# Kernel tuning notes

Measured on AMD Instinct MI355X. Metric: run time of the kernel, lower is better.

Reference implementation:

```python
import jax, jax.numpy as jnp
import numpy as np

B, N = 16, 512            # graphs per batch, nodes per graph
V, D_EMB = 100000, 64     # embedding table
F0 = 64                   # raw node feature width
H = 8                     # heads per layer
F_IN0 = F0 + D_EMB + 3    # 131 after concat(emb)+concat(user_emb)
O1, O2 = 128, 128         # f_out of layer 0 and 1
F_IN1 = H * O1            # 1024
EPS = 1e-5


def _xavier(key, shape):
    fan_in, fan_out = shape[-2], shape[-1]
    lim = float(np.sqrt(6.0 / (fan_in + fan_out)))
    return jax.random.uniform(key, shape, jnp.float32, -lim, lim)


def setup_inputs() -> dict:
    key = jax.random.key(0)
    ks = jax.random.split(key, 16)
    vertices = jax.random.randint(ks[0], (B, N), 0, V)
    adj = (jax.random.uniform(ks[1], (B, N, N)) < 0.1).astype(jnp.float32)
    adj = jnp.maximum(adj, jnp.eye(N, dtype=jnp.float32))  # self-loops: no empty softmax rows
    h = jax.random.normal(ks[2], (B, N, F0), jnp.float32)
    user_emb = jax.random.normal(ks[3], (B, N, 3), jnp.float32)
    emb_table = jax.random.normal(ks[4], (V, D_EMB), jnp.float32)
    return {
        "vertices": vertices, "adj": adj, "h": h, "user_emb": user_emb,
        "emb_table": emb_table,
        "norm1_w": jnp.ones((D_EMB,), jnp.float32), "norm1_b": jnp.zeros((D_EMB,), jnp.float32),
        "norm2_w": jnp.ones((3,), jnp.float32), "norm2_b": jnp.zeros((3,), jnp.float32),
        "w0": _xavier(ks[5], (H, F_IN0, O1)),
        "a_src0": _xavier(ks[6], (H, O1, 1)), "a_dst0": _xavier(ks[7], (H, O1, 1)),
        "w1": _xavier(ks[8], (H, F_IN1, O2)),
        "a_src1": _xavier(ks[9], (H, O2, 1)), "a_dst1": _xavier(ks[10], (H, O2, 1)),
    }


def _instance_norm(x, w, b):
    # torch InstanceNorm1d on x.transpose(1,2): normalize over node dim per (batch, channel)
    mu = jnp.mean(x, axis=1, keepdims=True)
    var = jnp.var(x, axis=1, keepdims=True)  # biased variance, as torch
    return (x - mu) * jax.lax.rsqrt(var + EPS) * w + b


def _gat_layer(h, adj, w, a_src, a_dst):
    # h: [b,n,f_in], w: [h,f_in,o]
    hp = jnp.einsum('bnf,hfo->bhno', h, w)            # h_prime
    t = jnp.tanh(hp)
    s = jnp.einsum('bhno,ho->bhn', t, a_src[..., 0])  # attn_src
    d = jnp.einsum('bhno,ho->bhn', t, a_dst[..., 0])  # attn_dst
    attn = s[:, :, :, None] + d[:, :, None, :]        # [b,h,n,n]
    attn = jnp.where(attn >= 0, attn, 0.2 * attn)     # leaky_relu(0.2)
    attn = jnp.where(adj[:, None, :, :] > 0, attn, -jnp.inf)
    attn = jax.nn.softmax(attn, axis=-1)              # (dropout is identity in eval)
    return jnp.einsum('bhnm,bhmo->bhno', attn, hp)


def reference(vertices, adj, h, user_emb, emb_table,
              norm1_w, norm1_b, norm2_w, norm2_b,
              w0, a_src0, a_dst0, w1, a_src1, a_dst1):
    emb = emb_table[vertices]                         # [b,n,D_EMB]
    emb = _instance_norm(emb, norm1_w, norm1_b)
    x = jnp.concatenate([h, emb], axis=2)
    ue = _instance_norm(user_emb, norm2_w, norm2_b)
    x = jnp.concatenate([x, ue], axis=2)              # [b,n,F_IN0]
    # layer 0 (not last): elu + head concat
    x = _gat_layer(x, adj, w0, a_src0, a_dst0)        # [b,H,n,O1]
    x = jax.nn.elu(jnp.transpose(x, (0, 2, 1, 3)).reshape(B, N, H * O1))
    # layer 1 (last): mean over heads
    x = _gat_layer(x, adj, w1, a_src1, a_dst1)        # [b,H,n,O2]
    x = jnp.mean(x, axis=1)                           # [b,n,O2]
    return jax.nn.log_softmax(x, axis=-1)
```

## Files before the change

### kernel.cpp

```cpp
#include <hip/hip_runtime.h>
#include <hip/hip_bf16.h>
#include <cmath>

#define B_  16
#define N_  512
#define H_  8
#define F0_ 64
#define DEMB_ 64
#define FIN0_ 131
#define KP0_ 192
#define O_  128
#define FIN1_ 1024
#define LOG2E_ 1.4426950408889634f

typedef __attribute__((ext_vector_type(4))) float f32x4;
typedef __attribute__((ext_vector_type(8))) short bf16x8;

__device__ inline ushort f2bf(float f) {
    union { float f; unsigned u; } x; x.f = f;
    unsigned r = x.u + 0x7fff + ((x.u >> 16) & 1);
    return (ushort)(r >> 16);
}
__device__ inline float bf2f(ushort u) {
    union { unsigned u; float f; } x; x.u = ((unsigned)u) << 16;
    return x.f;
}
__device__ inline float tanh_fast(float x) {
    x = fminf(fmaxf(x, -15.f), 15.f);
    float e = __expf(2.f * x);
    return (e - 1.f) * __frcp_rn(e + 1.f);
}

__global__ __launch_bounds__(256) void k_copy_h(const float* __restrict__ h,
                                                ushort* __restrict__ x0) {
    int i = blockIdx.x * 256 + threadIdx.x;
    int r = i >> 6, c = i & 63;
    x0[(size_t)r * KP0_ + c] = f2bf(h[i]);
    x0[(size_t)r * KP0_ + 128 + c] = 0;
}

__global__ __launch_bounds__(256) void k_emb_norm(const int* __restrict__ verts,
                                                  const float* __restrict__ table,
                                                  const float* __restrict__ w,
                                                  const float* __restrict__ bb,
                                                  ushort* __restrict__ x0) {
    int b = blockIdx.x >> 6, c = blockIdx.x & 63;
    int t = threadIdx.x;
    float vals[2], sum = 0.f, sq = 0.f;
#pragma unroll
    for (int i = 0; i < 2; ++i) {
        int n = t + i * 256;
        int vid = verts[b * N_ + n];
        float v = table[(size_t)vid * DEMB_ + c];
        vals[i] = v; sum += v; sq += v * v;
    }
    __shared__ float s0[256], s1[256];
    s0[t] = sum; s1[t] = sq; __syncthreads();
    for (int o = 128; o > 0; o >>= 1) {
        if (t < o) { s0[t] += s0[t + o]; s1[t] += s1[t + o]; }
        __syncthreads();
    }
    float mu = s0[0] * (1.f / N_);
    float var = s1[0] * (1.f / N_) - mu * mu;
    float inv = rsqrtf(var + 1e-5f);
    float ww = w[c], bv = bb[c];
#pragma unroll
    for (int i = 0; i < 2; ++i) {
        int n = t + i * 256;
        x0[((size_t)b * N_ + n) * KP0_ + 64 + c] = f2bf((vals[i] - mu) * inv * ww + bv);
    }
}

__global__ __launch_bounds__(256) void k_ue_norm(const float* __restrict__ ue,
                                                 const float* __restrict__ w,
                                                 const float* __restrict__ bb,
                                                 ushort* __restrict__ x0) {
    int b = blockIdx.x / 3, c = blockIdx.x % 3;
    int t = threadIdx.x;
    float vals[2], sum = 0.f, sq = 0.f;
#pragma unroll
    for (int i = 0; i < 2; ++i) {
        int n = t + i * 256;
        float v = ue[((size_t)b * N_ + n) * 3 + c];
        vals[i] = v; sum += v; sq += v * v;
    }
    __shared__ float s0[256], s1[256];
    s0[t] = sum; s1[t] = sq; __syncthreads();
    for (int o = 128; o > 0; o >>= 1) {
        if (t < o) { s0[t] += s0[t + o]; s1[t] += s1[t + o]; }
        __syncthreads();
    }
    float mu = s0[0] * (1.f / N_);
    float var = s1[0] * (1.f / N_) - mu * mu;
    float inv = rsqrtf(var + 1e-5f);
    float ww = w[c], bv = bb[c];
#pragma unroll
    for (int i = 0; i < 2; ++i) {
        int n = t + i * 256;
        x0[((size_t)b * N_ + n) * KP0_ + 128 + c] = f2bf((vals[i] - mu) * inv * ww + bv);
    }
}

__global__ __launch_bounds__(128) void k_wt_all(const float* __restrict__ w0,
                                                const float* __restrict__ w1,
                                                ushort* __restrict__ wt0,
                                                ushort* __restrict__ wt1) {
    int bid = blockIdx.x;
    int o = threadIdx.x;
    if (bid < 192) {
        int hh = bid / 24, kc = bid % 24;
        bf16x8 v;
#pragma unroll
        for (int j = 0; j < 8; ++j) {
            int k = kc * 8 + j;
            float f = (k < FIN0_) ? w0[((size_t)hh * FIN0_ + k) * 128 + o] : 0.f;
            v[j] = (short)f2bf(f);
        }
        *(bf16x8*)(wt0 + ((size_t)(hh * 128 + o)) * KP0_ + kc * 8) = v;
    } else {
        int b2 = bid - 192;
        int hh = b2 >> 7, kc = b2 & 127;
        bf16x8 v;
#pragma unroll
        for (int j = 0; j < 8; ++j) {
            int k = kc * 8 + j;
            float f = w1[((size_t)hh * FIN1_ + k) * 128 + o];
            v[j] = (short)f2bf(f);
        }
        *(bf16x8*)(wt1 + ((size_t)(hh * 128 + o)) * FIN1_ + kc * 8) = v;
    }
}

__global__ __launch_bounds__(256) void k_mask(const float* __restrict__ adj,
                                              unsigned long long* __restrict__ mask) {
    int gid = blockIdx.x * 256 + threadIdx.x;
    float v = adj[gid];
    unsigned long long m = __ballot(v > 0.f);
    if ((threadIdx.x & 63) == 0) mask[gid >> 6] = m;
}

template <int K>
__global__ __launch_bounds__(256, 2) void k_gemm(const ushort* __restrict__ A,
                                                 const ushort* __restrict__ Wt,
                                                 const float* __restrict__ asrc,
                                                 const float* __restrict__ adst,
                                                 ushort* __restrict__ hpT,
                                                 float* __restrict__ sout,
                                                 float* __restrict__ dout) {
    __shared__ ushort As[128 * 64];
    __shared__ ushort Bs[128 * 64];
    int bid = blockIdx.x;
    int hh = bid & 7;
    int mt = bid >> 3;
    int tid = threadIdx.x;
    int wid = tid >> 6, l = tid & 63;
    int wm = wid >> 1, wn = wid & 1;

    const ushort* Ab = A + (size_t)mt * 128 * K;
    const ushort* Wb = Wt + (size_t)hh * 128 * K;

    f32x4 acc[4][4];
#pragma unroll
    for (int m = 0; m < 4; ++m)
#pragma unroll
        for (int n = 0; n < 4; ++n) acc[m][n] = (f32x4){0.f, 0.f, 0.f, 0.f};

    int srow = tid >> 3;
    int segp = tid & 7;

    for (int kt = 0; kt < K / 64; ++kt) {
        int k0 = kt * 64;
#pragma unroll
        for (int it = 0; it < 4; ++it) {
            int row = it * 32 + srow;
            int segl = segp ^ (row & 7);
            size_t goff = (size_t)row * K + k0 + segl * 8;
            int loff = (it * 32 + wid * 8) * 64;
            __builtin_amdgcn_global_load_lds(
                (const __attribute__((address_space(1))) void*)(Ab + goff),
                (__attribute__((address_space(3))) void*)(As + loff), 16, 0, 0);
            __builtin_amdgcn_global_load_lds(
                (const __attribute__((address_space(1))) void*)(Wb + goff),
                (__attribute__((address_space(3))) void*)(Bs + loff), 16, 0, 0);
        }
        __syncthreads();

        int lr = l & 15;
        int kg = l >> 4;
#pragma unroll
        for (int kk = 0; kk < 2; ++kk) {
            int segl = kk * 4 + kg;
            bf16x8 a[4], b[4];
#pragma unroll
            for (int m = 0; m < 4; ++m) {
                int row = wm * 64 + m * 16 + lr;
                int sp = segl ^ (row & 7);
                a[m] = *(const bf16x8*)(As + row * 64 + sp * 8);
            }
#pragma unroll
            for (int n = 0; n < 4; ++n) {
                int row = wn * 64 + n * 16 + lr;
                int sp = segl ^ (row & 7);
                b[n] = *(const bf16x8*)(Bs + row * 64 + sp * 8);
            }
#pragma unroll
            for (int m = 0; m < 4; ++m)
#pragma unroll
                for (int n = 0; n < 4; ++n)
                    acc[m][n] = __builtin_amdgcn_mfma_f32_16x16x32_bf16(a[m], b[n], acc[m][n], 0, 0, 0);
        }
        __syncthreads();
    }

    int bb = mt >> 2;
    int n_in_b = (mt & 3) * 128;
    int bh = bb * H_ + hh;
    ushort* Hp = hpT + ((size_t)bh * 128) * 512;
#pragma unroll
    for (int m = 0; m < 4; ++m)
#pragma unroll
        for (int n = 0; n < 4; ++n) {
            int rr = wm * 64 + m * 16 + (l >> 4) * 4;
            int cc = wn * 64 + n * 16 + (l & 15);
            ushort4 v;
            v.x = f2bf(acc[m][n][0]);
            v.y = f2bf(acc[m][n][1]);
            v.z = f2bf(acc[m][n][2]);
            v.w = f2bf(acc[m][n][3]);
            *(ushort4*)(Hp + (size_t)cc * 512 + n_in_b + rr) = v;
        }

    float* sP = (float*)As;
    float* dP = sP + 256;
    float av[4], dv[4];
#pragma unroll
    for (int n = 0; n < 4; ++n) {
        int cc = wn * 64 + n * 16 + (l & 15);
        av[n] = asrc[hh * 128 + cc];
        dv[n] = adst[hh * 128 + cc];
    }
#pragma unroll
    for (int m = 0; m < 4; ++m)
#pragma unroll
        for (int j = 0; j < 4; ++j) {
            float sv = 0.f, dvv = 0.f;
#pragma unroll
            for (int n = 0; n < 4; ++n) {
                float th = tanh_fast(acc[m][n][j]);
                sv += th * av[n];
                dvv += th * dv[n];
            }
#pragma unroll
            for (int off = 1; off < 16; off <<= 1) {
                sv += __shfl_xor(sv, off);
                dvv += __shfl_xor(dvv, off);
            }
            if ((l & 15) == 0) {
                int rr = wm * 64 + m * 16 + (l >> 4) * 4 + j;
                sP[wn * 128 + rr] = sv;
                dP[wn * 128 + rr] = dvv;
            }
        }
    __syncthreads();
    if (tid < 128) {
        sout[(size_t)bh * 512 + n_in_b + tid] = (sP[tid] + sP[128 + tid]) * LOG2E_;
    } else {
        int r = tid - 128;
        dout[(size_t)bh * 512 + n_in_b + r] = (dP[r] + dP[128 + r]) * LOG2E_;
    }
}

template <bool L0>
__global__ __launch_bounds__(256, 2) void k_attn(const ushort* __restrict__ hpT,
                                                 const float* __restrict__ sbuf,
                                                 const float* __restrict__ dbuf,
                                                 const unsigned* __restrict__ mask32,
                                                 ushort* __restrict__ out) {
    __shared__ ushort Vbuf[128 * 64];
    __shared__ ushort Abuf[128 * 64];
    __shared__ float dsh[512];
    __shared__ float rsh[128];

    int bid = blockIdx.x;
    int xcd = bid & 7, idx = bid >> 3;
    int bh = xcd + 8 * (idx & 15);
    int tile = idx >> 4;
    int b = bh >> 3, hh = bh & 7;
    int n0 = tile * 128;
    int t = threadIdx.x;
    int wid = t >> 6, l = t & 63;
    int wm = wid >> 1, wn = wid & 1;
    int lr = l & 15, kg = l >> 4;

    const ushort* Vb = hpT + (size_t)bh * 128 * 512;

    int row = t >> 1, mh = t & 1;
    float sv = sbuf[(size_t)bh * 512 + n0 + row];
    unsigned mw[8];
#pragma unroll
    for (int c = 0; c < 8; ++c)
        mw[c] = mask32[((size_t)(b * 512 + n0 + row) << 4) + c * 2 + mh];

    dsh[t] = dbuf[(size_t)bh * 512 + t];
    dsh[256 + t] = dbuf[(size_t)bh * 512 + 256 + t];
    __syncthreads();

    f32x4 acc[4][4];
#pragma unroll
    for (int m = 0; m < 4; ++m)
#pragma unroll
        for (int n = 0; n < 4; ++n) acc[m][n] = (f32x4){0.f, 0.f, 0.f, 0.f};

    float rsum = 0.f;
    int srow = t >> 3, segp = t & 7;

#pragma unroll
    for (int c = 0; c < 8; ++c) {
        int m0 = c * 64;
#pragma unroll
        for (int it = 0; it < 4; ++it) {
            int rrow = it * 32 + srow;
            int segl = segp ^ (rrow & 7);
            __builtin_amdgcn_global_load_lds(
                (const __attribute__((address_space(1))) void*)(Vb + (size_t)rrow * 512 + m0 + segl * 8),
                (__attribute__((address_space(3))) void*)(Vbuf + (it * 32 + wid * 8) * 64),
                16, 0, 0);
        }

        const float* dp = dsh + m0 + mh * 32;
        unsigned mwc = mw[c];
#pragma unroll
        for (int j = 0; j < 4; ++j) {
            f32x4 da = *(const f32x4*)(dp + j * 8);
            f32x4 db2 = *(const f32x4*)(dp + j * 8 + 4);
            float ev[8];
#pragma unroll
            for (int q = 0; q < 8; ++q) {
                float dm = (q < 4) ? da[q] : db2[q - 4];
                float lg = sv + dm;
                lg = fmaxf(lg, 0.2f * lg);
                float e = ((mwc >> (j * 8 + q)) & 1) ? exp2f(lg) : 0.f;
                rsum += e;
                ev[q] = e;
            }
            unsigned p01, p23, p45, p67;
            asm("v_cvt_pk_bf16_f32 %0, %1, %2" : "=v"(p01) : "v"(ev[0]), "v"(ev[1]));
            asm("v_cvt_pk_bf16_f32 %0, %1, %2" : "=v"(p23) : "v"(ev[2]), "v"(ev[3]));
            asm("v_cvt_pk_bf16_f32 %0, %1, %2" : "=v"(p45) : "v"(ev[4]), "v"(ev[5]));
            asm("v_cvt_pk_bf16_f32 %0, %1, %2" : "=v"(p67) : "v"(ev[6]), "v"(ev[7]));
            int s = mh * 4 + j;
            int phys = s ^ (row & 7);
            uint4 pk4 = {p01, p23, p45, p67};
            *(uint4*)((char*)Abuf + row * 128 + phys * 16) = pk4;
        }
        __syncthreads();

#pragma unroll
        for (int kk = 0; kk < 2; ++kk) {
            int s = kk * 4 + kg;
            bf16x8 a[4], bfr[4];
#pragma unroll
            for (int m = 0; m < 4; ++m) {
                int rw = wm * 64 + m * 16 + lr;
                int sp = s ^ (rw & 7);
                a[m] = *(const bf16x8*)(Vbuf + rw * 64 + sp * 8);
            }
#pragma unroll
            for (int n = 0; n < 4; ++n) {
                int rw = wn * 64 + n * 16 + lr;
                int sp = s ^ (rw & 7);
                bfr[n] = *(const bf16x8*)(Abuf + rw * 64 + sp * 8);
            }
#pragma unroll
            for (int m = 0; m < 4; ++m)
#pragma unroll
                for (int n = 0; n < 4; ++n)
                    acc[m][n] = __builtin_amdgcn_mfma_f32_16x16x32_bf16(a[m], bfr[n], acc[m][n], 0, 0, 0);
        }
        __syncthreads();
    }

    rsum += __shfl_xor(rsum, 1);
    if ((t & 1) == 0) rsh[row] = rsum;
    __syncthreads();

#pragma unroll
    for (int n = 0; n < 4; ++n) {
        int nn = wn * 64 + n * 16 + lr;
        float ri = __frcp_rn(rsh[nn]);
        size_t orow;
        if (L0)
            orow = ((size_t)(b * 512 + n0 + nn)) * FIN1_ + hh * 128;
        else
            orow = ((size_t)bh * 512 + n0 + nn) * 128;
#pragma unroll
        for (int m = 0; m < 4; ++m) {
            int o0 = wm * 64 + m * 16 + kg * 4;
            f32x4 v = acc[m][n];
            ushort4 w;
            float f0 = v[0] * ri, f1 = v[1] * ri, f2 = v[2] * ri, f3 = v[3] * ri;
            if (L0) {
                f0 = (f0 > 0.f) ? f0 : expm1f(f0);
                f1 = (f1 > 0.f) ? f1 : expm1f(f1);
                f2 = (f2 > 0.f) ? f2 : expm1f(f2);
                f3 = (f3 > 0.f) ? f3 : expm1f(f3);
            }
            w.x = f2bf(f0); w.y = f2bf(f1); w.z = f2bf(f2); w.w = f2bf(f3);
            *(ushort4*)(out + orow + o0) = w;
        }
    }
}

__global__ __launch_bounds__(128) void k_out(const ushort* __restrict__ o1,
                                             float* __restrict__ out) {
    int row = blockIdx.x;
    int b = row >> 9, n = row & 511;
    int t = threadIdx.x;
    float v = 0.f;
#pragma unroll
    for (int hh = 0; hh < H_; ++hh)
        v += bf2f(o1[((size_t)(b * H_ + hh) * N_ + n) * O_ + t]);
    v *= 0.125f;
    float m = v;
#pragma unroll
    for (int off = 32; off > 0; off >>= 1) m = fmaxf(m, __shfl_down(m, off));
    __shared__ float red[4];
    if ((t & 63) == 0) red[t >> 6] = m;
    __syncthreads();
    float rm = fmaxf(red[0], red[1]);
    float e = __expf(v - rm);
    float ss = e;
#pragma unroll
    for (int off = 32; off > 0; off >>= 1) ss += __shfl_down(ss, off);
    if ((t & 63) == 0) red[2 + (t >> 6)] = ss;
    __syncthreads();
    float rs2 = red[2] + red[3];
    out[(size_t)row * O_ + t] = v - rm - logf(rs2);
}

extern "C" void kernel_launch(void* const* d_in, const int* in_sizes, int n_in,
                              void* d_out, int out_size, void* d_ws, size_t ws_size,
                              hipStream_t stream) {
    const int*   verts = (const int*)d_in[0];
    const float* adj   = (const float*)d_in[1];
    const float* h     = (const float*)d_in[2];
    const float* ue    = (const float*)d_in[3];
    const float* table = (const float*)d_in[4];
    const float* n1w   = (const float*)d_in[5];
    const float* n1b   = (const float*)d_in[6];
    const float* n2w   = (const float*)d_in[7];
    const float* n2b   = (const float*)d_in[8];
    const float* w0    = (const float*)d_in[9];
    const float* as0   = (const float*)d_in[10];
    const float* ad0   = (const float*)d_in[11];
    const float* w1    = (const float*)d_in[12];
    const float* as1   = (const float*)d_in[13];
    const float* ad1   = (const float*)d_in[14];
    float* out = (float*)d_out;

    ushort* x0p  = (ushort*)d_ws;
    ushort* wt0  = x0p + 1572864;
    ushort* wt1  = wt0 + 196608;
    ushort* hpT  = wt1 + 1048576;
    ushort* x1bf = hpT + 8388608;
    ushort* o1   = x1bf + 8388608;
    unsigned long long* mask = (unsigned long long*)(o1 + 8388608);
    float* sb = (float*)(mask + 65536);
    float* db = sb + 65536;

    hipLaunchKernelGGL(k_copy_h,   dim3(2048), dim3(256), 0, stream, h, x0p);
    hipLaunchKernelGGL(k_emb_norm, dim3(1024), dim3(256), 0, stream, verts, table, n1w, n1b, x0p);
    hipLaunchKernelGGL(k_ue_norm,  dim3(48),   dim3(256), 0, stream, ue, n2w, n2b, x0p);
    hipLaunchKernelGGL(k_wt_all,   dim3(1216), dim3(128), 0, stream, w0, w1, wt0, wt1);
    hipLaunchKernelGGL(k_mask,     dim3(16384), dim3(256), 0, stream, adj, mask);

    hipLaunchKernelGGL((k_gemm<KP0_>), dim3(512), dim3(256), 0, stream,
                       x0p, wt0, as0, ad0, hpT, sb, db);
    hipLaunchKernelGGL((k_attn<true>), dim3(512), dim3(256), 0, stream,
                       hpT, sb, db, (const unsigned*)mask, x1bf);

    hipLaunchKernelGGL((k_gemm<FIN1_>), dim3(512), dim3(256), 0, stream,
                       x1bf, wt1, as1, ad1, hpT, sb, db);
    hipLaunchKernelGGL((k_attn<false>), dim3(512), dim3(256), 0, stream,
                       hpT, sb, db, (const unsigned*)mask, o1);

    hipLaunchKernelGGL(k_out, dim3(8192), dim3(128), 0, stream, o1, out);
}
```

Before: 142.1 us.

## Fuse preprocessing kernels, remap GEMM blocks, halve attention query tile

Merges the five preprocessing launches (feature copy, embedding norm, user-emb norm, weight transpose, mask build) into one kernel that branches on block index, removing launch gaps. The GEMM block order now groups M-tiles per XCD so neighbouring blocks share a head's weight tile. Attention drops to 64 query rows per block with four threads per row, doubling the grid to 1024 blocks for better occupancy and load balance. The cost is that each attention block reloads the V tile for half as many queries, and the fused preprocess kernel is a single large grid with divergent block roles.

After: 117.2 us. -17.6%, faster.

```diff
diff --git a/kernel.cpp b/kernel.cpp
--- a/kernel.cpp
+++ b/kernel.cpp
@@ -31,112 +31,110 @@
     return (e - 1.f) * __frcp_rn(e + 1.f);
 }
 
-__global__ __launch_bounds__(256) void k_copy_h(const float* __restrict__ h,
-                                                ushort* __restrict__ x0) {
-    int i = blockIdx.x * 256 + threadIdx.x;
-    int r = i >> 6, c = i & 63;
-    x0[(size_t)r * KP0_ + c] = f2bf(h[i]);
-    x0[(size_t)r * KP0_ + 128 + c] = 0;
-}
-
-__global__ __launch_bounds__(256) void k_emb_norm(const int* __restrict__ verts,
-                                                  const float* __restrict__ table,
-                                                  const float* __restrict__ w,
-                                                  const float* __restrict__ bb,
-                                                  ushort* __restrict__ x0) {
-    int b = blockIdx.x >> 6, c = blockIdx.x & 63;
+__global__ __launch_bounds__(256) void k_pre(const float* __restrict__ h,
+                                             const int* __restrict__ verts,
+                                             const float* __restrict__ table,
+                                             const float* __restrict__ n1w,
+                                             const float* __restrict__ n1b,
+                                             const float* __restrict__ ue,
+                                             const float* __restrict__ n2w,
+                                             const float* __restrict__ n2b,
+                                             const float* __restrict__ w0,
+                                             const float* __restrict__ w1,
+                                             const float* __restrict__ adj,
+                                             ushort* __restrict__ x0,
+                                             ushort* __restrict__ wt0,
+                                             ushort* __restrict__ wt1,
+                                             unsigned long long* __restrict__ mask) {
+    __shared__ float s0[256], s1[256];
+    int bid = blockIdx.x;
     int t = threadIdx.x;
-    float vals[2], sum = 0.f, sq = 0.f;
-#pragma unroll
-    for (int i = 0; i < 2; ++i) {
-        int n = t + i * 256;
-        int vid = verts[b * N_ + n];
-        float v = table[(size_t)vid * DEMB_ + c];
-        vals[i] = v; sum += v; sq += v * v;
-    }
-    __shared__ float s0[256], s1[256];
-    s0[t] = sum; s1[t] = sq; __syncthreads();
-    for (int o = 128; o > 0; o >>= 1) {
-        if (t < o) { s0[t] += s0[t + o]; s1[t] += s1[t + o]; }
-        __syncthreads();
-    }
-    float mu = s0[0] * (1.f / N_);
-    float var = s1[0] * (1.f / N_) - mu * mu;
-    float inv = rsqrtf(var + 1e-5f);
-    float ww = w[c], bv = bb[c];
-#pragma unroll
-    for (int i = 0; i < 2; ++i) {
-        int n = t + i * 256;
-        x0[((size_t)b * N_ + n) * KP0_ + 64 + c] = f2bf((vals[i] - mu) * inv * ww + bv);
-    }
-}
-
-__global__ __launch_bounds__(256) void k_ue_norm(const float* __restrict__ ue,
-                                                 const float* __restrict__ w,
-                                                 const float* __restrict__ bb,
-                                                 ushort* __restrict__ x0) {
-    int b = blockIdx.x / 3, c = blockIdx.x % 3;
-    int t = threadIdx.x;
-    float vals[2], sum = 0.f, sq = 0.f;
-#pragma unroll
-    for (int i = 0; i < 2; ++i) {
-        int n = t + i * 256;
-        float v = ue[((size_t)b * N_ + n) * 3 + c];
-        vals[i] = v; sum += v; sq += v * v;
-    }
-    __shared__ float s0[256], s1[256];
-    s0[t] = sum; s1[t] = sq; __syncthreads();
-    for (int o = 128; o > 0; o >>= 1) {
-        if (t < o) { s0[t] += s0[t + o]; s1[t] += s1[t + o]; }
-        __syncthreads();
-    }
-    float mu = s0[0] * (1.f / N_);
-    float var = s1[0] * (1.f / N_) - mu * mu;
-    float inv = rsqrtf(var + 1e-5f);
-    float ww = w[c], bv = bb[c];
-#pragma unroll
-    for (int i = 0; i < 2; ++i) {
-        int n = t + i * 256;
-        x0[((size_t)b * N_ + n) * KP0_ + 128 + c] = f2bf((vals[i] - mu) * inv * ww + bv);
-    }
-}
-
-__global__ __launch_bounds__(128) void k_wt_all(const float* __restrict__ w0,
-                                                const float* __restrict__ w1,
-                                                ushort* __restrict__ wt0,
-                                                ushort* __restrict__ wt1) {
-    int bid = blockIdx.x;
-    int o = threadIdx.x;
-    if (bid < 192) {
-        int hh = bid / 24, kc = bid % 24;
-        bf16x8 v;
-#pragma unroll
-        for (int j = 0; j < 8; ++j) {
-            int k = kc * 8 + j;
-            float f = (k < FIN0_) ? w0[((size_t)hh * FIN0_ + k) * 128 + o] : 0.f;
-            v[j] = (short)f2bf(f);
-        }
-        *(bf16x8*)(wt0 + ((size_t)(hh * 128 + o)) * KP0_ + kc * 8) = v;
+
+    if (bid < 2048) {
+        int i = bid * 256 + t;
+        int r = i >> 6, c = i & 63;
+        x0[(size_t)r * KP0_ + c] = f2bf(h[i]);
+        if (c >= 3) x0[(size_t)r * KP0_ + 128 + c] = 0;
+    } else if (bid < 3072) {
+        int b2 = bid - 2048;
+        int b = b2 >> 6, c = b2 & 63;
+        float vals[2], sum = 0.f, sq = 0.f;
+#pragma unroll
+        for (int i = 0; i < 2; ++i) {
+            int n = t + i * 256;
+            int vid = verts[b * N_ + n];
+            float v = table[(size_t)vid * DEMB_ + c];
+            vals[i] = v; sum += v; sq += v * v;
+        }
+        s0[t] = sum; s1[t] = sq; __syncthreads();
+        for (int o = 128; o > 0; o >>= 1) {
+            if (t < o) { s0[t] += s0[t + o]; s1[t] += s1[t + o]; }
+            __syncthreads();
+        }
+        float mu = s0[0] * (1.f / N_);
+        float var = s1[0] * (1.f / N_) - mu * mu;
+        float inv = rsqrtf(var + 1e-5f);
+        float ww = n1w[c], bv = n1b[c];
+#pragma unroll
+        for (int i = 0; i < 2; ++i) {
+            int n = t + i * 256;
+            x0[((size_t)b * N_ + n) * KP0_ + 64 + c] = f2bf((vals[i] - mu) * inv * ww + bv);
+        }
+    } else if (bid < 3120) {
+        int b3 = bid - 3072;
+        int b = b3 / 3, c = b3 % 3;
+        float vals[2], sum = 0.f, sq = 0.f;
+#pragma unroll
+        for (int i = 0; i < 2; ++i) {
+            int n = t + i * 256;
+            float v = ue[((size_t)b * N_ + n) * 3 + c];
+            vals[i] = v; sum += v; sq += v * v;
+        }
+        s0[t] = sum; s1[t] = sq; __syncthreads();
+        for (int o = 128; o > 0; o >>= 1) {
+            if (t < o) { s0[t] += s0[t + o]; s1[t] += s1[t + o]; }
+            __syncthreads();
+        }
+        float mu = s0[0] * (1.f / N_);
+        float var = s1[0] * (1.f / N_) - mu * mu;
+        float inv = rsqrtf(var + 1e-5f);
+        float ww = n2w[c], bv = n2b[c];
+#pragma unroll
+        for (int i = 0; i < 2; ++i) {
+            int n = t + i * 256;
+            x0[((size_t)b * N_ + n) * KP0_ + 128 + c] = f2bf((vals[i] - mu) * inv * ww + bv);
+        }
+    } else if (bid < 3728) {
+        int ob = (bid - 3120) * 2 + (t >> 7);
+        int o = t & 127;
+        if (ob < 192) {
+            int hh = ob / 24, kc = ob % 24;
+            bf16x8 v;
+#pragma unroll
+            for (int j = 0; j < 8; ++j) {
+                int k = kc * 8 + j;
+                float f = (k < FIN0_) ? w0[((size_t)hh * FIN0_ + k) * 128 + o] : 0.f;
+                v[j] = (short)f2bf(f);
+            }
+            *(bf16x8*)(wt0 + ((size_t)(hh * 128 + o)) * KP0_ + kc * 8) = v;
+        } else {
+            int b2 = ob - 192;
+            int hh = b2 >> 7, kc = b2 & 127;
+            bf16x8 v;
+#pragma unroll
+            for (int j = 0; j < 8; ++j) {
+                int k = kc * 8 + j;
+                float f = w1[((size_t)hh * FIN1_ + k) * 128 + o];
+                v[j] = (short)f2bf(f);
+            }
+            *(bf16x8*)(wt1 + ((size_t)(hh * 128 + o)) * FIN1_ + kc * 8) = v;
+        }
     } else {
-        int b2 = bid - 192;
-        int hh = b2 >> 7, kc = b2 & 127;
-        bf16x8 v;
-#pragma unroll
-        for (int j = 0; j < 8; ++j) {
-            int k = kc * 8 + j;
-            float f = w1[((size_t)hh * FIN1_ + k) * 128 + o];
-            v[j] = (short)f2bf(f);
-        }
-        *(bf16x8*)(wt1 + ((size_t)(hh * 128 + o)) * FIN1_ + kc * 8) = v;
-    }
-}
-
-__global__ __launch_bounds__(256) void k_mask(const float* __restrict__ adj,
-                                              unsigned long long* __restrict__ mask) {
-    int gid = blockIdx.x * 256 + threadIdx.x;
-    float v = adj[gid];
-    unsigned long long m = __ballot(v > 0.f);
-    if ((threadIdx.x & 63) == 0) mask[gid >> 6] = m;
+        int gid = (bid - 3728) * 256 + t;
+        float v = adj[gid];
+        unsigned long long m = __ballot(v > 0.f);
+        if ((t & 63) == 0) mask[gid >> 6] = m;
+    }
 }
 
 template <int K>
@@ -150,8 +148,9 @@
     __shared__ ushort As[128 * 64];
     __shared__ ushort Bs[128 * 64];
     int bid = blockIdx.x;
-    int hh = bid & 7;
-    int mt = bid >> 3;
+    int idx = bid >> 3;
+    int mt = (bid & 7) + 8 * (idx & 7);
+    int hh = idx >> 3;
     int tid = threadIdx.x;
     int wid = tid >> 6, l = tid & 63;
     int wm = wid >> 1, wn = wid & 1;
@@ -277,16 +276,16 @@
                                                  const unsigned* __restrict__ mask32,
                                                  ushort* __restrict__ out) {
     __shared__ ushort Vbuf[128 * 64];
-    __shared__ ushort Abuf[128 * 64];
+    __shared__ ushort Abuf[64 * 64];
     __shared__ float dsh[512];
-    __shared__ float rsh[128];
+    __shared__ float rsh[64];
 
     int bid = blockIdx.x;
     int xcd = bid & 7, idx = bid >> 3;
     int bh = xcd + 8 * (idx & 15);
     int tile = idx >> 4;
     int b = bh >> 3, hh = bh & 7;
-    int n0 = tile * 128;
+    int n0 = tile * 64;
     int t = threadIdx.x;
     int wid = t >> 6, l = t & 63;
     int wm = wid >> 1, wn = wid & 1;
@@ -294,22 +293,23 @@
 
     const ushort* Vb = hpT + (size_t)bh * 128 * 512;
 
-    int row = t >> 1, mh = t & 1;
+    int row = t >> 2, q4 = t & 3;
     float sv = sbuf[(size_t)bh * 512 + n0 + row];
+    int msh = (q4 & 1) * 16;
     unsigned mw[8];
 #pragma unroll
     for (int c = 0; c < 8; ++c)
-        mw[c] = mask32[((size_t)(b * 512 + n0 + row) << 4) + c * 2 + mh];
+        mw[c] = mask32[((size_t)(b * 512 + n0 + row) << 4) + c * 2 + (q4 >> 1)];
 
     dsh[t] = dbuf[(size_t)bh * 512 + t];
     dsh[256 + t] = dbuf[(size_t)bh * 512 + 256 + t];
     __syncthreads();
 
-    f32x4 acc[4][4];
+    f32x4 acc[4][2];
 #pragma unroll
     for (int m = 0; m < 4; ++m)
 #pragma unroll
-        for (int n = 0; n < 4; ++n) acc[m][n] = (f32x4){0.f, 0.f, 0.f, 0.f};
+        for (int n = 0; n < 2; ++n) acc[m][n] = (f32x4){0.f, 0.f, 0.f, 0.f};
 
     float rsum = 0.f;
     int srow = t >> 3, segp = t & 7;
@@ -327,10 +327,10 @@
                 16, 0, 0);
         }
 
-        const float* dp = dsh + m0 + mh * 32;
-        unsigned mwc = mw[c];
-#pragma unroll
-        for (int j = 0; j < 4; ++j) {
+        const float* dp = dsh + m0 + q4 * 16;
+        unsigned mwc = mw[c] >> msh;
+#pragma unroll
+        for (int j = 0; j < 2; ++j) {
             f32x4 da = *(const f32x4*)(dp + j * 8);
             f32x4 db2 = *(const f32x4*)(dp + j * 8 + 4);
             float ev[8];
@@ -348,7 +348,7 @@
             asm("v_cvt_pk_bf16_f32 %0, %1, %2" : "=v"(p23) : "v"(ev[2]), "v"(ev[3]));
             asm("v_cvt_pk_bf16_f32 %0, %1, %2" : "=v"(p45) : "v"(ev[4]), "v"(ev[5]));
             asm("v_cvt_pk_bf16_f32 %0, %1, %2" : "=v"(p67) : "v"(ev[6]), "v"(ev[7]));
-            int s = mh * 4 + j;
+            int s = q4 * 2 + j;
             int phys = s ^ (row & 7);
             uint4 pk4 = {p01, p23, p45, p67};
             *(uint4*)((char*)Abuf + row * 128 + phys * 16) = pk4;
@@ -358,7 +358,7 @@
 #pragma unroll
         for (int kk = 0; kk < 2; ++kk) {
             int s = kk * 4 + kg;
-            bf16x8 a[4], bfr[4];
+            bf16x8 a[4], bfr[2];
 #pragma unroll
             for (int m = 0; m < 4; ++m) {
                 int rw = wm * 64 + m * 16 + lr;
@@ -366,27 +366,28 @@
                 a[m] = *(const bf16x8*)(Vbuf + rw * 64 + sp * 8);
             }
 #pragma unroll
-            for (int n = 0; n < 4; ++n) {
-                int rw = wn * 64 + n * 16 + lr;
+            for (int n = 0; n < 2; ++n) {
+                int rw = wn * 32 + n * 16 + lr;
                 int sp = s ^ (rw & 7);
                 bfr[n] = *(const bf16x8*)(Abuf + rw * 64 + sp * 8);
             }
 #pragma unroll
             for (int m = 0; m < 4; ++m)
 #pragma unroll
-                for (int n = 0; n < 4; ++n)
+                for (int n = 0; n < 2; ++n)
                     acc[m][n] = __builtin_amdgcn_mfma_f32_16x16x32_bf16(a[m], bfr[n], acc[m][n], 0, 0, 0);
         }
         __syncthreads();
     }
 
     rsum += __shfl_xor(rsum, 1);
-    if ((t & 1) == 0) rsh[row] = rsum;
+    rsum += __shfl_xor(rsum, 2);
+    if (q4 == 0) rsh[row] = rsum;
     __syncthreads();
 
 #pragma unroll
-    for (int n = 0; n < 4; ++n) {
-        int nn = wn * 64 + n * 16 + lr;
+    for (int n = 0; n < 2; ++n) {
+        int nn = wn * 32 + n * 16 + lr;
         float ri = __frcp_rn(rsh[nn]);
         size_t orow;
         if (L0)
@@ -468,20 +469,18 @@
     float* sb = (float*)(mask + 65536);
     float* db = sb + 65536;
 
-    hipLaunchKernelGGL(k_copy_h,   dim3(2048), dim3(256), 0, stream, h, x0p);
-    hipLaunchKernelGGL(k_emb_norm, dim3(1024), dim3(256), 0, stream, verts, table, n1w, n1b, x0p);
-    hipLaunchKernelGGL(k_ue_norm,  dim3(48),   dim3(256), 0, stream, ue, n2w, n2b, x0p);
-    hipLaunchKernelGGL(k_wt_all,   dim3(1216), dim3(128), 0, stream, w0, w1, wt0, wt1);
-    hipLaunchKernelGGL(k_mask,     dim3(16384), dim3(256), 0, stream, adj, mask);
+    hipLaunchKernelGGL(k_pre, dim3(20112), dim3(256), 0, stream,
+                       h, verts, table, n1w, n1b, ue, n2w, n2b, w0, w1, adj,
+                       x0p, wt0, wt1, mask);
 
     hipLaunchKernelGGL((k_gemm<KP0_>), dim3(512), dim3(256), 0, stream,
                        x0p, wt0, as0, ad0, hpT, sb, db);
-    hipLaunchKernelGGL((k_attn<true>), dim3(512), dim3(256), 0, stream,
+    hipLaunchKernelGGL((k_attn<true>), dim3(1024), dim3(256), 0, stream,
                        hpT, sb, db, (const unsigned*)mask, x1bf);
 
     hipLaunchKernelGGL((k_gemm<FIN1_>), dim3(512), dim3(256), 0, stream,
                        x1bf, wt1, as1, ad1, hpT, sb, db);
-    hipLaunchKernelGGL((k_attn<false>), dim3(512), dim3(256), 0, stream,
+    hipLaunchKernelGGL((k_attn<false>), dim3(1024), dim3(256), 0, stream,
                        hpT, sb, db, (const unsigned*)mask, o1);
 
     hipLaunchKernelGGL(k_out, dim3(8192), dim3(128), 0, stream, o1, out);
```
